# Kernel tuning notes

Measured on AMD Instinct MI355X. Metric: run time of the kernel, lower is better.

## Reference

```python
import jax, jax.numpy as jnp
import numpy as np

B, T, DM, H, DK, DV = 2, 2048, 1024, 16, 64, 64


def setup_inputs() -> dict:
    key = jax.random.key(0)
    k = jax.random.split(key, 7)
    std_k = np.float32(1.0 / np.sqrt(DK))
    std_v = np.float32(1.0 / np.sqrt(DV))
    return {
        "xq": jax.random.normal(k[0], (B, T, DM), jnp.float32),
        "xk": jax.random.normal(k[1], (B, T, DM), jnp.float32),
        "xv": jax.random.normal(k[2], (B, T, DM), jnp.float32),
        "mask": jnp.ones((B, T), jnp.float32),  # padding mask: 1 = keep
        "w_q": jax.random.normal(k[3], (H, DM, DK), jnp.float32) * std_k,
        "w_k": jax.random.normal(k[4], (H, DM, DK), jnp.float32) * std_k,
        "w_v": jax.random.normal(k[5], (H, DM, DV), jnp.float32) * std_v,
        "w_o": jax.random.normal(k[6], (H * DV, DM), jnp.float32) * np.float32(1.0 / np.sqrt(H * DV)),
        "b_o": jnp.zeros((DM,), jnp.float32),
    }


def reference(xq, xk, xv, mask, w_q, w_k, w_v, w_o, b_o):
    d_k = w_q.shape[-1]
    # per-head projections: [B,T,DM] x [H,DM,DK] -> [B,H,T,DK]
    q = jnp.einsum('bsd,hdk->bhsk', xq, w_q)
    kk = jnp.einsum('btd,hdk->bhtk', xk, w_k)
    v = jnp.einsum('btd,hdv->bhtv', xv, w_v)
    # NOTE: source divides by d_k (not sqrt(d_k)) -- kept faithful
    scores = jnp.einsum('bhsk,bhtk->bhst', q, kk) / jnp.float32(d_k)
    # _padding_mask: multiply by mask broadcast over key dim, then any exact
    # zero (masked OR coincidentally zero score) becomes -inf -- kept faithful
    masked = scores * mask[:, None, None, :]
    scores = jnp.where(masked == 0.0, -jnp.inf, masked)
    attn = jax.nn.softmax(scores, axis=-1)
    out = jnp.einsum('bhst,bhtv->bhsv', attn, v)  # [B,H,T,DV]
    b, h, t, dv = out.shape
    concat = out.transpose(0, 2, 1, 3).reshape(b, t, h * dv)
    return concat @ w_o + b_o
```

## Files before the change

kernel.cpp:

```cpp
#include <hip/hip_runtime.h>
#include <hip/hip_bf16.h>


typedef __attribute__((ext_vector_type(8))) short short8;
typedef __attribute__((ext_vector_type(4))) short short4v;
typedef __attribute__((ext_vector_type(4))) float f32x4;
typedef __attribute__((ext_vector_type(4))) int i32x4;

__device__ __forceinline__ short f2bf(float f) {
  union { float f; unsigned u; } v; v.f = f;
  unsigned r = v.u + 0x7FFFu + ((v.u >> 16) & 1u);
  return (short)(r >> 16);
}

#define GLD_LDS(g, l) __builtin_amdgcn_global_load_lds( \
    (const __attribute__((address_space(1))) void*)(g), \
    (__attribute__((address_space(3))) void*)(l), 16, 0, 0)

__global__ __launch_bounds__(256) void prep_all(
    const float* __restrict__ xq, const float* __restrict__ xk,
    const float* __restrict__ xv, const float* __restrict__ wq,
    const float* __restrict__ wk, const float* __restrict__ wv,
    const float* __restrict__ wo,
    short* __restrict__ Xb, short* __restrict__ Wall, short* __restrict__ Wot)
{
  const int bx = blockIdx.x, tid = threadIdx.x;
  __shared__ float Lt[64][65];
  if (bx < 6144) {
    int z = bx >> 11;
    const float* x = z == 0 ? xq : (z == 1 ? xk : xv);
    size_t i = ((size_t)(bx & 2047) * 256 + tid) * 8;
    f32x4 f0 = *(const f32x4*)(x + i);
    f32x4 f1 = *(const f32x4*)(x + i + 4);
    short8 s;
#pragma unroll
    for (int j = 0; j < 4; j++) { s[j] = f2bf(f0[j]); s[4 + j] = f2bf(f1[j]); }
    *(short8*)(Xb + (size_t)z * 4194304 + i) = s;
  } else if (bx < 6912) {
    int bz = bx - 6144;
    int z = bz >> 8, inner = bz & 255;
    const float* w = z == 0 ? wq : (z == 1 ? wk : wv);
    short* Wt = Wall + (size_t)z * 1048576;
    int h = inner >> 4, d0 = (inner & 15) * 64;
#pragma unroll
    for (int it = 0; it < 4; it++) {
      int e = tid + it * 256;
      int dl = e >> 4, k4 = (e & 15) * 4;
      f32x4 v = *(const f32x4*)(w + ((size_t)(h * 1024 + d0 + dl) * 64) + k4);
#pragma unroll
      for (int j = 0; j < 4; j++) Lt[dl][k4 + j] = v[j];
    }
    __syncthreads();
#pragma unroll
    for (int it = 0; it < 4; it++) {
      int e = tid + it * 256;
      int kl = e >> 4, dq = e & 15;
      short4v s;
#pragma unroll
      for (int j = 0; j < 4; j++) s[j] = f2bf(Lt[dq * 4 + j][kl]);
      *(short4v*)(Wt + (size_t)(h * 64 + kl) * 1024 + d0 + dq * 4) = s;
    }
  } else {
    int bz = bx - 6912;
    int k0 = (bz >> 4) * 64, n0 = (bz & 15) * 64;
#pragma unroll
    for (int it = 0; it < 4; it++) {
      int e = tid + it * 256;
      int kl = e >> 4, n4 = (e & 15) * 4;
      f32x4 v = *(const f32x4*)(wo + (size_t)(k0 + kl) * 1024 + n0 + n4);
#pragma unroll
      for (int j = 0; j < 4; j++) Lt[kl][n4 + j] = v[j];
    }
    __syncthreads();
#pragma unroll
    for (int it = 0; it < 4; it++) {
      int e = tid + it * 256;
      int nl = e >> 4, kq = e & 15;
      short4v s;
#pragma unroll
      for (int j = 0; j < 4; j++) s[j] = f2bf(Lt[kq * 4 + j][nl]);
      *(short4v*)(Wot + (size_t)(n0 + nl) * 1024 + k0 + kq * 4) = s;
    }
  }
}

__global__ __launch_bounds__(256) void proj_qkv2(
    const short* __restrict__ Xb, const short* __restrict__ Wall,
    short* __restrict__ Qb, short* __restrict__ Kt2, short* __restrict__ Vt2)
{
  const int z = blockIdx.z;
  const short* X  = Xb   + (size_t)z * 4194304;
  const short* Wt = Wall + (size_t)z * 1048576;

  const int t0 = blockIdx.x * 128;
  const int n0 = blockIdx.y * 128;
  const int tid = threadIdx.x, w = tid >> 6, lane = tid & 63;
  const int c = lane & 15, q4 = lane >> 4;
  const int wn = (w & 1) * 64, wt = (w >> 1) * 64;
  const int srow = lane >> 2, scol = (lane & 3) * 8;

  __shared__ __align__(16) short Al[128 * 32];
  __shared__ __align__(16) short Bl[128 * 32];

  f32x4 acc[4][4] = {};

  for (int k0 = 0; k0 < 1024; k0 += 32) {
#pragma unroll
    for (int i = 0; i < 2; i++) {
      int rg = (w * 2 + i) * 16;
      GLD_LDS(Wt + (size_t)(n0 + rg + srow) * 1024 + k0 + scol, Al + rg * 32);
      GLD_LDS(X  + (size_t)(t0 + rg + srow) * 1024 + k0 + scol, Bl + rg * 32);
    }
    __syncthreads();
    short8 a[4], bfr[4];
#pragma unroll
    for (int i = 0; i < 4; i++)
      a[i] = *(const short8*)(Al + (wn + i * 16 + c) * 32 + q4 * 8);
#pragma unroll
    for (int j = 0; j < 4; j++)
      bfr[j] = *(const short8*)(Bl + (wt + j * 16 + c) * 32 + q4 * 8);
#pragma unroll
    for (int i = 0; i < 4; i++)
#pragma unroll
      for (int j = 0; j < 4; j++)
        acc[i][j] = __builtin_amdgcn_mfma_f32_16x16x32_bf16(a[i], bfr[j], acc[i][j], 0, 0, 0);
    __syncthreads();
  }

#pragma unroll
  for (int i = 0; i < 4; i++)
#pragma unroll
    for (int j = 0; j < 4; j++) {
      int n = n0 + wn + i * 16 + q4 * 4;
      int trow = t0 + wt + j * 16 + c;
      int b = trow >> 11, t = trow & 2047;
      int h = n >> 6, cc = n & 63;
      int bh = b * 16 + h;
      f32x4 v = acc[i][j];
      short4v pk;
#pragma unroll
      for (int r = 0; r < 4; r++) pk[r] = f2bf(v[r]);
      if (z == 0) {
        *(short4v*)(Qb + (size_t)(bh * 2048 + t) * 64 + cc) = pk;
      } else if (z == 1) {
        int t5 = t & 31, s_ = t5 >> 4, c_ = t5 & 15;
        size_t base = (size_t)bh * 131072 + (t >> 5) * 2048;
#pragma unroll
        for (int r = 0; r < 4; r++) {
          int dv = cc + r;
          Kt2[base + ((s_ * 2 + (dv >> 5)) * 16 + c_) * 32 + ((dv >> 3) & 3) * 8 + (dv & 7)] = pk[r];
        }
      } else {
        int t5 = t & 31;
        int kp = ((t5 >> 2) & 3) * 8 + ((t5 >> 4) & 1) * 4 + (t5 & 3);
        size_t base = (size_t)bh * 131072 + (t >> 5) * 2048;
#pragma unroll
        for (int r = 0; r < 4; r++)
          Vt2[base + (size_t)(cc + r) * 32 + kp] = pk[r];
      }
    }
}

__global__ __launch_bounds__(256, 2) void attn8(
    const short* __restrict__ Qb, const short* __restrict__ Kt2,
    const short* __restrict__ Vt2, const float* __restrict__ mask,
    short* __restrict__ AO)
{
  const int bh = blockIdx.x;
  const int tblk = blockIdx.y;
  const int b = bh >> 4, h = bh & 15;
  const short* Qh = Qb  + (size_t)bh * 131072;
  const short* Kh = Kt2 + (size_t)bh * 131072;
  const short* Vh = Vt2 + (size_t)bh * 131072;

  const int tid = threadIdx.x, w = tid >> 6, lane = tid & 63;
  const int c = lane & 15, q4 = lane >> 4;
  const int qrow0 = tblk * 128 + w * 32;

  __shared__ __align__(16) short KV[3][4096];
  __shared__ __align__(16) float Ml[2048];

  const int ch = c * 4 + q4;
  const int rdo = (ch ^ ((ch >> 3) & 3)) * 8;
  const int sch = (lane ^ ((lane >> 3) & 3)) * 8;

  {
    f32x4 m0 = *(const f32x4*)(mask + b * 2048 + tid * 8);
    f32x4 m1 = *(const f32x4*)(mask + b * 2048 + tid * 8 + 4);
    *(f32x4*)(&Ml[tid * 8]) = m0;
    *(f32x4*)(&Ml[tid * 8 + 4]) = m1;
  }

  short8 qa[2][2];
#pragma unroll
  for (int u = 0; u < 2; u++)
#pragma unroll
    for (int dc = 0; dc < 2; dc++)
      qa[u][dc] = *(const short8*)(Qh + (size_t)(qrow0 + u * 16 + c) * 64 + dc * 32 + q4 * 8);

  f32x4 acc[2][4] = {};
  float l[2] = {0.f, 0.f};
  const float LOG2E_64 = 1.44269504088896f * 0.015625f;

  const int g0 = w * 2;

#define STAGE(BI, T) do { \
    const short* sb = (g0 < 4) ? (Kh + (size_t)(T) * 2048 + g0 * 512) \
                               : (Vh + (size_t)(T) * 2048 + (g0 - 4) * 512); \
    GLD_LDS(sb + sch,        &KV[BI][g0 * 512]); \
    GLD_LDS(sb + 512 + sch,  &KV[BI][g0 * 512 + 512]); \
  } while (0)

#define BODY(BI, TT) do { \
    const short* Kb = &KV[BI][0]; \
    short8 kf[2][2], va[4]; \
    _Pragma("unroll") \
    for (int s = 0; s < 2; s++) \
      _Pragma("unroll") \
      for (int dc = 0; dc < 2; dc++) \
        kf[s][dc] = *(const short8*)(Kb + (s * 2 + dc) * 512 + rdo); \
    _Pragma("unroll") \
    for (int vs = 0; vs < 4; vs++) \
      va[vs] = *(const short8*)(Kb + (4 + vs) * 512 + rdo); \
    f32x4 st[2][2] = {}; \
    _Pragma("unroll") \
    for (int u = 0; u < 2; u++) \
      _Pragma("unroll") \
      for (int s = 0; s < 2; s++) { \
        st[u][s] = __builtin_amdgcn_mfma_f32_16x16x32_bf16(kf[s][0], qa[u][0], st[u][s], 0, 0, 0); \
        st[u][s] = __builtin_amdgcn_mfma_f32_16x16x32_bf16(kf[s][1], qa[u][1], st[u][s], 0, 0, 0); \
      } \
    f32x4 cm[2], cb[2]; \
    _Pragma("unroll") \
    for (int s = 0; s < 2; s++) { \
      f32x4 mk = *(const f32x4*)(&Ml[(TT) * 32 + q4 * 4 + s * 16]); \
      cm[s] = mk * LOG2E_64; \
      cb[s] = (mk - 1.0f) * 240.0f; \
    } \
    _Pragma("unroll") \
    for (int u = 0; u < 2; u++) { \
      unsigned pkd[2][2]; \
      _Pragma("unroll") \
      for (int s = 0; s < 2; s++) { \
        float e0 = __builtin_amdgcn_exp2f(st[u][s][0] * cm[s][0] + cb[s][0]); \
        float e1 = __builtin_amdgcn_exp2f(st[u][s][1] * cm[s][1] + cb[s][1]); \
        float e2 = __builtin_amdgcn_exp2f(st[u][s][2] * cm[s][2] + cb[s][2]); \
        float e3 = __builtin_amdgcn_exp2f(st[u][s][3] * cm[s][3] + cb[s][3]); \
        l[u] += (e0 + e1) + (e2 + e3); \
        union { float f; unsigned u; } a0, a1, a2, a3; \
        a0.f = e0; a1.f = e1; a2.f = e2; a3.f = e3; \
        pkd[s][0] = __builtin_amdgcn_perm(a1.u + 0x8000u, a0.u + 0x8000u, 0x07060302u); \
        pkd[s][1] = __builtin_amdgcn_perm(a3.u + 0x8000u, a2.u + 0x8000u, 0x07060302u); \
      } \
      union { i32x4 i; short8 s; } pb; \
      pb.i[0] = (int)pkd[0][0]; pb.i[1] = (int)pkd[0][1]; \
      pb.i[2] = (int)pkd[1][0]; pb.i[3] = (int)pkd[1][1]; \
      _Pragma("unroll") \
      for (int vs = 0; vs < 4; vs++) \
        acc[u][vs] = __builtin_amdgcn_mfma_f32_16x16x32_bf16(va[vs], pb.s, acc[u][vs], 0, 0, 0); \
    } \
  } while (0)

  __syncthreads();
  asm volatile("s_waitcnt vmcnt(0)" ::: "memory");
  __builtin_amdgcn_sched_barrier(0);
  STAGE(0, 0);
  STAGE(1, 1);

  int bi = 0;
  for (int t = 0; t < 62; ++t) {
    asm volatile("s_waitcnt vmcnt(2)" ::: "memory");
    __builtin_amdgcn_sched_barrier(0);
    __builtin_amdgcn_s_barrier();
    __builtin_amdgcn_sched_barrier(0);
    int si = bi + 2; if (si >= 3) si -= 3;
    STAGE(si, t + 2);
    BODY(bi, t);
    bi = (bi + 1 == 3) ? 0 : bi + 1;
  }
  asm volatile("s_waitcnt vmcnt(2)" ::: "memory");
  __builtin_amdgcn_sched_barrier(0);
  __builtin_amdgcn_s_barrier();
  __builtin_amdgcn_sched_barrier(0);
  BODY(bi, 62);
  asm volatile("s_waitcnt vmcnt(0)" ::: "memory");
  __builtin_amdgcn_sched_barrier(0);
  __builtin_amdgcn_s_barrier();
  __builtin_amdgcn_sched_barrier(0);
  BODY(0, 63);
#undef STAGE
#undef BODY

#pragma unroll
  for (int u = 0; u < 2; u++) {
    float lu = l[u];
    lu += __shfl_xor(lu, 16);
    lu += __shfl_xor(lu, 32);
    float inv = 1.0f / lu;
    size_t row = (size_t)b * 2048 + qrow0 + u * 16 + c;
#pragma unroll
    for (int vs = 0; vs < 4; vs++) {
      f32x4 v = acc[u][vs];
      short4v pk;
#pragma unroll
      for (int r = 0; r < 4; r++) pk[r] = f2bf(v[r] * inv);
      *(short4v*)(AO + row * 1024 + h * 64 + vs * 16 + q4 * 4) = pk;
    }
  }
}

__global__ __launch_bounds__(256) void out_proj2(
    const short* __restrict__ AO, const short* __restrict__ Wot,
    const float* __restrict__ bo, float* __restrict__ out)
{
  const int t0 = blockIdx.x * 128;
  const int n0 = blockIdx.y * 128;
  const int tid = threadIdx.x, w = tid >> 6, lane = tid & 63;
  const int c = lane & 15, q4 = lane >> 4;
  const int wn = (w & 1) * 64, wt = (w >> 1) * 64;
  const int srow = lane >> 2, scol = (lane & 3) * 8;

  __shared__ __align__(16) short Al[128 * 32];
  __shared__ __align__(16) short Bl[128 * 32];

  f32x4 acc[4][4] = {};

  for (int k0 = 0; k0 < 1024; k0 += 32) {
#pragma unroll
    for (int i = 0; i < 2; i++) {
      int rg = (w * 2 + i) * 16;
      GLD_LDS(Wot + (size_t)(n0 + rg + srow) * 1024 + k0 + scol, Al + rg * 32);
      GLD_LDS(AO  + (size_t)(t0 + rg + srow) * 1024 + k0 + scol, Bl + rg * 32);
    }
    __syncthreads();
    short8 a[4], bfr[4];
#pragma unroll
    for (int i = 0; i < 4; i++)
      a[i] = *(const short8*)(Al + (wn + i * 16 + c) * 32 + q4 * 8);
#pragma unroll
    for (int j = 0; j < 4; j++)
      bfr[j] = *(const short8*)(Bl + (wt + j * 16 + c) * 32 + q4 * 8);
#pragma unroll
    for (int i = 0; i < 4; i++)
#pragma unroll
      for (int j = 0; j < 4; j++)
        acc[i][j] = __builtin_amdgcn_mfma_f32_16x16x32_bf16(a[i], bfr[j], acc[i][j], 0, 0, 0);
    __syncthreads();
  }

#pragma unroll
  for (int i = 0; i < 4; i++)
#pragma unroll
    for (int j = 0; j < 4; j++) {
      int n = n0 + wn + i * 16 + q4 * 4;
      int trow = t0 + wt + j * 16 + c;
      f32x4 v = acc[i][j] + *(const f32x4*)(bo + n);
      *(f32x4*)(out + (size_t)trow * 1024 + n) = v;
    }
}

extern "C" void kernel_launch(void* const* d_in, const int* in_sizes, int n_in,
                              void* d_out, int out_size, void* d_ws, size_t ws_size,
                              hipStream_t stream)
{
  (void)in_sizes; (void)n_in; (void)out_size; (void)ws_size;
  const float* xq   = (const float*)d_in[0];
  const float* xk   = (const float*)d_in[1];
  const float* xv   = (const float*)d_in[2];
  const float* mask = (const float*)d_in[3];
  const float* wq   = (const float*)d_in[4];
  const float* wk   = (const float*)d_in[5];
  const float* wv   = (const float*)d_in[6];
  const float* wo   = (const float*)d_in[7];
  const float* bo   = (const float*)d_in[8];
  float* out = (float*)d_out;

  char* ws = (char*)d_ws;
  short* Wall = (short*)(ws + (size_t)0);
  short* Wot  = (short*)(ws + ((size_t)6 << 20));
  short* Xb   = (short*)(ws + ((size_t)8 << 20));
  short* AO   = (short*)(ws + ((size_t)8 << 20));
  short* Qb   = (short*)(ws + ((size_t)32 << 20));
  short* Kt2  = (short*)(ws + ((size_t)40 << 20));
  short* Vt2  = (short*)(ws + ((size_t)48 << 20));

  prep_all<<<7168, 256, 0, stream>>>(xq, xk, xv, wq, wk, wv, wo, Xb, Wall, Wot);
  proj_qkv2<<<dim3(32, 8, 3), 256, 0, stream>>>(Xb, Wall, Qb, Kt2, Vt2);
  attn8<<<dim3(32, 16), 256, 0, stream>>>(Qb, Kt2, Vt2, mask, AO);
  out_proj2<<<dim3(32, 8), 256, 0, stream>>>(AO, Wot, bo, out);
}
```

Baseline: 224.5 us.

## Software-pipeline QK^T with softmax/PV across tiles in attention kernel

Restructures the attention loop so that the QK^T MFMAs for tile t+1 are issued before the softmax and PV of tile t, using ping-pong score and V registers. Mask coefficients are precomputed into two LDS arrays, and the bf16 packing now uses v_cvt_pk_bf16_f32 instead of a manual round and perm. The K-transpose store in the projection kernel becomes one vectorized short4 write instead of four scalar writes. The aim is better overlap of MFMA and exp work; the cost is more register pressure and extra LDS, which could hurt the two-blocks-per-CU occupancy.

New measurement: 222.1 us. About the same (-1.1%).

```diff
diff --git a/kernel.cpp b/kernel.cpp
--- a/kernel.cpp
+++ b/kernel.cpp
@@ -145,11 +145,9 @@
       } else if (z == 1) {
         int t5 = t & 31, s_ = t5 >> 4, c_ = t5 & 15;
         size_t base = (size_t)bh * 131072 + (t >> 5) * 2048;
-#pragma unroll
-        for (int r = 0; r < 4; r++) {
-          int dv = cc + r;
-          Kt2[base + ((s_ * 2 + (dv >> 5)) * 16 + c_) * 32 + ((dv >> 3) & 3) * 8 + (dv & 7)] = pk[r];
-        }
+        size_t off = base + ((s_ * 2 + (cc >> 5)) * 16 + c_) * 32 +
+                     ((cc >> 3) & 3) * 8 + (cc & 7);
+        *(short4v*)(Kt2 + off) = pk;
       } else {
         int t5 = t & 31;
         int kp = ((t5 >> 2) & 3) * 8 + ((t5 >> 4) & 1) * 4 + (t5 & 3);
@@ -161,7 +159,7 @@
     }
 }
 
-__global__ __launch_bounds__(256, 2) void attn8(
+__global__ __launch_bounds__(256, 2) void attn9(
     const short* __restrict__ Qb, const short* __restrict__ Kt2,
     const short* __restrict__ Vt2, const float* __restrict__ mask,
     short* __restrict__ AO)
@@ -178,17 +176,21 @@
   const int qrow0 = tblk * 128 + w * 32;
 
   __shared__ __align__(16) short KV[3][4096];
-  __shared__ __align__(16) float Ml[2048];
+  __shared__ __align__(16) float cmL[2048];
+  __shared__ __align__(16) float cbL[2048];
 
   const int ch = c * 4 + q4;
   const int rdo = (ch ^ ((ch >> 3) & 3)) * 8;
   const int sch = (lane ^ ((lane >> 3) & 3)) * 8;
 
   {
+    const float LOG2E_64c = 1.44269504088896f * 0.015625f;
     f32x4 m0 = *(const f32x4*)(mask + b * 2048 + tid * 8);
     f32x4 m1 = *(const f32x4*)(mask + b * 2048 + tid * 8 + 4);
-    *(f32x4*)(&Ml[tid * 8]) = m0;
-    *(f32x4*)(&Ml[tid * 8 + 4]) = m1;
+    *(f32x4*)(&cmL[tid * 8])     = m0 * LOG2E_64c;
+    *(f32x4*)(&cmL[tid * 8 + 4]) = m1 * LOG2E_64c;
+    *(f32x4*)(&cbL[tid * 8])     = (m0 - 1.0f) * 240.0f;
+    *(f32x4*)(&cbL[tid * 8 + 4]) = (m1 - 1.0f) * 240.0f;
   }
 
   short8 qa[2][2];
@@ -200,7 +202,6 @@
 
   f32x4 acc[2][4] = {};
   float l[2] = {0.f, 0.f};
-  const float LOG2E_64 = 1.44269504088896f * 0.015625f;
 
   const int g0 = w * 2;
 
@@ -211,9 +212,9 @@
     GLD_LDS(sb + 512 + sch,  &KV[BI][g0 * 512 + 512]); \
   } while (0)
 
-#define BODY(BI, TT) do { \
+#define QK(BI, ST, VA) do { \
     const short* Kb = &KV[BI][0]; \
-    short8 kf[2][2], va[4]; \
+    short8 kf[2][2]; \
     _Pragma("unroll") \
     for (int s = 0; s < 2; s++) \
       _Pragma("unroll") \
@@ -221,75 +222,99 @@
         kf[s][dc] = *(const short8*)(Kb + (s * 2 + dc) * 512 + rdo); \
     _Pragma("unroll") \
     for (int vs = 0; vs < 4; vs++) \
-      va[vs] = *(const short8*)(Kb + (4 + vs) * 512 + rdo); \
-    f32x4 st[2][2] = {}; \
+      VA[vs] = *(const short8*)(Kb + (4 + vs) * 512 + rdo); \
     _Pragma("unroll") \
     for (int u = 0; u < 2; u++) \
       _Pragma("unroll") \
       for (int s = 0; s < 2; s++) { \
-        st[u][s] = __builtin_amdgcn_mfma_f32_16x16x32_bf16(kf[s][0], qa[u][0], st[u][s], 0, 0, 0); \
-        st[u][s] = __builtin_amdgcn_mfma_f32_16x16x32_bf16(kf[s][1], qa[u][1], st[u][s], 0, 0, 0); \
+        f32x4 z = {}; \
+        z = __builtin_amdgcn_mfma_f32_16x16x32_bf16(kf[s][0], qa[u][0], z, 0, 0, 0); \
+        ST[u][s] = __builtin_amdgcn_mfma_f32_16x16x32_bf16(kf[s][1], qa[u][1], z, 0, 0, 0); \
       } \
+  } while (0)
+
+#define SMPV(ST, VA, TT) do { \
     f32x4 cm[2], cb[2]; \
     _Pragma("unroll") \
     for (int s = 0; s < 2; s++) { \
-      f32x4 mk = *(const f32x4*)(&Ml[(TT) * 32 + q4 * 4 + s * 16]); \
-      cm[s] = mk * LOG2E_64; \
-      cb[s] = (mk - 1.0f) * 240.0f; \
+      cm[s] = *(const f32x4*)(&cmL[(TT) * 32 + q4 * 4 + s * 16]); \
+      cb[s] = *(const f32x4*)(&cbL[(TT) * 32 + q4 * 4 + s * 16]); \
     } \
     _Pragma("unroll") \
     for (int u = 0; u < 2; u++) { \
       unsigned pkd[2][2]; \
       _Pragma("unroll") \
       for (int s = 0; s < 2; s++) { \
-        float e0 = __builtin_amdgcn_exp2f(st[u][s][0] * cm[s][0] + cb[s][0]); \
-        float e1 = __builtin_amdgcn_exp2f(st[u][s][1] * cm[s][1] + cb[s][1]); \
-        float e2 = __builtin_amdgcn_exp2f(st[u][s][2] * cm[s][2] + cb[s][2]); \
-        float e3 = __builtin_amdgcn_exp2f(st[u][s][3] * cm[s][3] + cb[s][3]); \
+        float e0 = __builtin_amdgcn_exp2f(ST[u][s][0] * cm[s][0] + cb[s][0]); \
+        float e1 = __builtin_amdgcn_exp2f(ST[u][s][1] * cm[s][1] + cb[s][1]); \
+        float e2 = __builtin_amdgcn_exp2f(ST[u][s][2] * cm[s][2] + cb[s][2]); \
+        float e3 = __builtin_amdgcn_exp2f(ST[u][s][3] * cm[s][3] + cb[s][3]); \
         l[u] += (e0 + e1) + (e2 + e3); \
-        union { float f; unsigned u; } a0, a1, a2, a3; \
-        a0.f = e0; a1.f = e1; a2.f = e2; a3.f = e3; \
-        pkd[s][0] = __builtin_amdgcn_perm(a1.u + 0x8000u, a0.u + 0x8000u, 0x07060302u); \
-        pkd[s][1] = __builtin_amdgcn_perm(a3.u + 0x8000u, a2.u + 0x8000u, 0x07060302u); \
+        unsigned p01, p23; \
+        asm("v_cvt_pk_bf16_f32 %0, %1, %2" : "=v"(p01) : "v"(e0), "v"(e1)); \
+        asm("v_cvt_pk_bf16_f32 %0, %1, %2" : "=v"(p23) : "v"(e2), "v"(e3)); \
+        pkd[s][0] = p01; pkd[s][1] = p23; \
       } \
       union { i32x4 i; short8 s; } pb; \
       pb.i[0] = (int)pkd[0][0]; pb.i[1] = (int)pkd[0][1]; \
       pb.i[2] = (int)pkd[1][0]; pb.i[3] = (int)pkd[1][1]; \
       _Pragma("unroll") \
       for (int vs = 0; vs < 4; vs++) \
-        acc[u][vs] = __builtin_amdgcn_mfma_f32_16x16x32_bf16(va[vs], pb.s, acc[u][vs], 0, 0, 0); \
+        acc[u][vs] = __builtin_amdgcn_mfma_f32_16x16x32_bf16(VA[vs], pb.s, acc[u][vs], 0, 0, 0); \
     } \
   } while (0)
+
+  f32x4 stA[2][2], stB[2][2];
+  short8 vaA[4], vaB[4];
 
   __syncthreads();
   asm volatile("s_waitcnt vmcnt(0)" ::: "memory");
   __builtin_amdgcn_sched_barrier(0);
   STAGE(0, 0);
   STAGE(1, 1);
-
-  int bi = 0;
-  for (int t = 0; t < 62; ++t) {
-    asm volatile("s_waitcnt vmcnt(2)" ::: "memory");
+  asm volatile("s_waitcnt vmcnt(2) lgkmcnt(0)" ::: "memory");
+  __builtin_amdgcn_sched_barrier(0);
+  __builtin_amdgcn_s_barrier();
+  __builtin_amdgcn_sched_barrier(0);
+  STAGE(2, 2);
+  QK(0, stA, vaA);
+
+  int bs = 0;
+  for (int ii = 0; ii < 31; ++ii) {
+    const int t = 2 * ii;
+    asm volatile("s_waitcnt vmcnt(2) lgkmcnt(0)" ::: "memory");
     __builtin_amdgcn_sched_barrier(0);
     __builtin_amdgcn_s_barrier();
     __builtin_amdgcn_sched_barrier(0);
-    int si = bi + 2; if (si >= 3) si -= 3;
-    STAGE(si, t + 2);
-    BODY(bi, t);
-    bi = (bi + 1 == 3) ? 0 : bi + 1;
-  }
-  asm volatile("s_waitcnt vmcnt(2)" ::: "memory");
+    if (t + 3 < 64) STAGE(bs, t + 3);
+    {
+      int bn = bs + 1; if (bn == 3) bn = 0;
+      QK(bn, stB, vaB);
+    }
+    SMPV(stA, vaA, t);
+    bs = bs + 1; if (bs == 3) bs = 0;
+    asm volatile("s_waitcnt vmcnt(2) lgkmcnt(0)" ::: "memory");
+    __builtin_amdgcn_sched_barrier(0);
+    __builtin_amdgcn_s_barrier();
+    __builtin_amdgcn_sched_barrier(0);
+    if (t + 4 < 64) STAGE(bs, t + 4);
+    {
+      int bn = bs + 1; if (bn == 3) bn = 0;
+      QK(bn, stA, vaA);
+    }
+    SMPV(stB, vaB, t + 1);
+    bs = bs + 1; if (bs == 3) bs = 0;
+  }
+  asm volatile("s_waitcnt vmcnt(0) lgkmcnt(0)" ::: "memory");
   __builtin_amdgcn_sched_barrier(0);
   __builtin_amdgcn_s_barrier();
   __builtin_amdgcn_sched_barrier(0);
-  BODY(bi, 62);
-  asm volatile("s_waitcnt vmcnt(0)" ::: "memory");
-  __builtin_amdgcn_sched_barrier(0);
-  __builtin_amdgcn_s_barrier();
-  __builtin_amdgcn_sched_barrier(0);
-  BODY(0, 63);
+  QK(0, stB, vaB);
+  SMPV(stA, vaA, 62);
+  SMPV(stB, vaB, 63);
 #undef STAGE
-#undef BODY
+#undef QK
+#undef SMPV
 
 #pragma unroll
   for (int u = 0; u < 2; u++) {
@@ -386,6 +411,6 @@
 
   prep_all<<<7168, 256, 0, stream>>>(xq, xk, xv, wq, wk, wv, wo, Xb, Wall, Wot);
   proj_qkv2<<<dim3(32, 8, 3), 256, 0, stream>>>(Xb, Wall, Qb, Kt2, Vt2);
-  attn8<<<dim3(32, 16), 256, 0, stream>>>(Qb, Kt2, Vt2, mask, AO);
+  attn9<<<dim3(32, 16), 256, 0, stream>>>(Qb, Kt2, Vt2, mask, AO);
   out_proj2<<<dim3(32, 8), 256, 0, stream>>>(AO, Wot, bo, out);
 }
```
